# Optimization experiments

Measured on AMD Instinct MI355X. Metric: run time of the kernel, lower is better.

Reference implementation:

```python
import jax, jax.numpy as jnp
from jax import lax
import numpy as np

POOLED_H = 7
POOLED_W = 7
SPATIAL_SCALE = 0.0625


def setup_inputs() -> dict:
    key = jax.random.key(0)
    kf, kx1, ky1, kw, kh = jax.random.split(key, 5)
    B, H, W, C = 1, 64, 64, 512
    N = 512
    img_h, img_w = H / SPATIAL_SCALE, W / SPATIAL_SCALE
    feat = jax.random.normal(kf, (B, H, W, C), dtype=jnp.float32)
    # rois: (batch_idx, x1, y1, x2, y2) in image coordinates, boxes inside image
    x1 = jax.random.uniform(kx1, (N,), minval=0.0, maxval=img_w * 0.8)
    y1 = jax.random.uniform(ky1, (N,), minval=0.0, maxval=img_h * 0.8)
    bw = jax.random.uniform(kw, (N,), minval=16.0, maxval=img_w * 0.5)
    bh = jax.random.uniform(kh, (N,), minval=16.0, maxval=img_h * 0.5)
    x2 = jnp.clip(x1 + bw, 0.0, img_w - 1.0)
    y2 = jnp.clip(y1 + bh, 0.0, img_h - 1.0)
    bidx = jnp.zeros((N,), dtype=jnp.float32)
    rois = jnp.stack([bidx, x1, y1, x2, y2], axis=1).astype(jnp.float32)
    return {"feat": feat, "rois": rois}


def _roi_pool(feat, rois, pooled_h, pooled_w, spatial_scale):
    B, H, W, C = feat.shape
    N = rois.shape[0]
    # max extent of a single bin (Caffe: hend-hstart <= bin_size + 2 <= H/pooled_h + 2)
    MBH = int(np.ceil(H / pooled_h)) + 2
    MBW = int(np.ceil(W / pooled_w)) + 2

    roi_batch = rois[:, 0].astype(jnp.int32)
    start_w = jnp.round(rois[:, 1] * spatial_scale).astype(jnp.int32)
    start_h = jnp.round(rois[:, 2] * spatial_scale).astype(jnp.int32)
    end_w = jnp.round(rois[:, 3] * spatial_scale).astype(jnp.int32)
    end_h = jnp.round(rois[:, 4] * spatial_scale).astype(jnp.int32)
    roi_h = jnp.maximum(end_h - start_h + 1, 1).astype(jnp.float32)
    roi_w = jnp.maximum(end_w - start_w + 1, 1).astype(jnp.float32)
    bin_h = roi_h / pooled_h  # [N] float
    bin_w = roi_w / pooled_w

    ar_h = jnp.arange(MBH)
    ar_w = jnp.arange(MBW)

    def pool_one_bin(bin_idx):
        ph = bin_idx // pooled_w
        pw = bin_idx % pooled_w

        def per_roi(b, sh, sw, bh_, bw_):
            hstart = jnp.clip(jnp.floor(ph * bh_).astype(jnp.int32) + sh, 0, H)
            hend = jnp.clip(jnp.ceil((ph + 1) * bh_).astype(jnp.int32) + sh, 0, H)
            wstart = jnp.clip(jnp.floor(pw * bw_).astype(jnp.int32) + sw, 0, W)
            wend = jnp.clip(jnp.ceil((pw + 1) * bw_).astype(jnp.int32) + sw, 0, W)
            empty = (hend <= hstart) | (wend <= wstart)
            # fixed-size window covering the bin; clamp start so slice stays in-bounds
            s_h = jnp.clip(hstart, 0, H - MBH)
            s_w = jnp.clip(wstart, 0, W - MBW)
            fmap = lax.dynamic_index_in_dim(feat, b, axis=0, keepdims=False)  # [H,W,C]
            patch = lax.dynamic_slice(fmap, (s_h, s_w, 0), (MBH, MBW, C))  # [MBH,MBW,C]
            rows = s_h + ar_h
            cols = s_w + ar_w
            valid = ((rows >= hstart) & (rows < hend))[:, None] & ((cols >= wstart) & (cols < wend))[None, :]
            neg = jnp.array(-jnp.inf, patch.dtype)
            mx = jnp.max(jnp.where(valid[:, :, None], patch, neg), axis=(0, 1))  # [C]
            return jnp.where(empty, jnp.zeros_like(mx), mx)

        return jax.vmap(per_roi)(roi_batch, start_h, start_w, bin_h, bin_w)  # [N,C]

    out = lax.map(pool_one_bin, jnp.arange(pooled_h * pooled_w))  # [PH*PW, N, C]
    out = out.transpose(1, 0, 2).reshape(N, pooled_h, pooled_w, C)
    return out


def reference(feat, rois):
    return _roi_pool(feat, rois, POOLED_H, POOLED_W, SPATIAL_SCALE)
```

## Files before the change

kernel.cpp:

```cpp
#include <hip/hip_runtime.h>
#include <cmath>

#define PH 7
#define PW 7
#define FH 64
#define FW 64
#define CC 512
#define SCALE 0.0625f

typedef float f32x4 __attribute__((ext_vector_type(4)));

static __device__ __forceinline__ f32x4 vmax4(f32x4 a, f32x4 b) {
    f32x4 r;
    r.x = fmaxf(a.x, b.x); r.y = fmaxf(a.y, b.y);
    r.z = fmaxf(a.z, b.z); r.w = fmaxf(a.w, b.w);
    return r;
}

__global__ __launch_bounds__(512) void sort_rois_kernel(
        const float* __restrict__ rois, int N, int* __restrict__ perm) {
    __shared__ int base[64];
    __shared__ int cur[64];
    int t = threadIdx.x;
    if (t < 64) { base[t] = 0; cur[t] = 0; }
    __syncthreads();
    int b = -1;
    if (t < N) {
        const float* r = rois + (size_t)t * 5;
        int sh = (int)rintf(r[2] * SCALE);
        b = min(max(sh, 0), FH - 1);
        atomicAdd(&base[b], 1);
    }
    __syncthreads();
    if (t == 0) {
        int acc = 0;
        for (int i = 0; i < 64; ++i) { int c = base[i]; base[i] = acc; acc += c; }
    }
    __syncthreads();
    if (t < N) {
        int pos = base[b] + atomicAdd(&cur[b], 1);
        perm[pos] = t;
    }
}

__global__ __launch_bounds__(256) void roi_pool_kernel(
        const float* __restrict__ feat,
        const float* __restrict__ rois,
        const int* __restrict__ perm,
        float* __restrict__ out,
        int nBins) {
    int p = blockIdx.x;
    int nwg = gridDim.x;
    int q = nwg >> 3, rr = nwg & 7;
    int xcd = p & 7, o = p >> 3;
    int L = (xcd < rr ? xcd * (q + 1) : rr * (q + 1) + (xcd - rr) * q) + o;

    int tid = L * 256 + (int)threadIdx.x;
    int bin = tid >> 6;
    int lane = tid & 63;
    if (bin >= nBins) return;

    int s   = bin / (PH * PW);
    int rem = bin - s * (PH * PW);
    int ph  = rem / PW;
    int pw  = rem - ph * PW;
    int n   = perm[s];

    const float* r = rois + (size_t)n * 5;
    int bidx = (int)r[0];
    int sw = (int)rintf(r[1] * SCALE);
    int sh = (int)rintf(r[2] * SCALE);
    int ew = (int)rintf(r[3] * SCALE);
    int eh = (int)rintf(r[4] * SCALE);

    float roi_h = fmaxf((float)(eh - sh + 1), 1.0f);
    float roi_w = fmaxf((float)(ew - sw + 1), 1.0f);
    float bh = roi_h * (1.0f / 7.0f);
    float bw = roi_w * (1.0f / 7.0f);

    int hstart = min(max((int)floorf((float)ph * bh) + sh, 0), FH);
    int hend   = min(max((int)ceilf((float)(ph + 1) * bh) + sh, 0), FH);
    int wstart = min(max((int)floorf((float)pw * bw) + sw, 0), FW);
    int wend   = min(max((int)ceilf((float)(pw + 1) * bw) + sw, 0), FW);
    bool empty = (hend <= hstart) || (wend <= wstart);

    f32x4 mxA = { -INFINITY, -INFINITY, -INFINITY, -INFINITY };
    f32x4 mxB = mxA;

    if (!empty) {
        const int W = wend - wstart;
        int cells = (hend - hstart) * W;
        const float* ptr = feat + (size_t)bidx * (FH * FW * CC)
                         + (size_t)hstart * (FW * CC) + (size_t)wstart * CC
                         + (size_t)lane * 4;
        const int stepWrap = (FW - W + 1) * CC;
        int cw = W;

#define ADV() do { if (--cw == 0) { ptr += stepWrap; cw = W; } else ptr += CC; } while (0)

        while (cells >= 4) {
            const float* q0 = ptr; ADV();
            const float* q1 = ptr; ADV();
            const float* q2 = ptr; ADV();
            const float* q3 = ptr; ADV();
            f32x4 a0 = *(const f32x4*)q0;        f32x4 b0 = *(const f32x4*)(q0 + 256);
            f32x4 a1 = *(const f32x4*)q1;        f32x4 b1 = *(const f32x4*)(q1 + 256);
            f32x4 a2 = *(const f32x4*)q2;        f32x4 b2 = *(const f32x4*)(q2 + 256);
            f32x4 a3 = *(const f32x4*)q3;        f32x4 b3 = *(const f32x4*)(q3 + 256);
            a0 = vmax4(a0, a1); a2 = vmax4(a2, a3);
            b0 = vmax4(b0, b1); b2 = vmax4(b2, b3);
            mxA = vmax4(mxA, vmax4(a0, a2));
            mxB = vmax4(mxB, vmax4(b0, b2));
            cells -= 4;
        }
        while (cells > 0) {
            const float* q0 = ptr; ADV();
            f32x4 a0 = *(const f32x4*)q0;
            f32x4 b0 = *(const f32x4*)(q0 + 256);
            mxA = vmax4(mxA, a0);
            mxB = vmax4(mxB, b0);
            --cells;
        }
#undef ADV
    } else {
        mxA = (f32x4){0.f, 0.f, 0.f, 0.f};
        mxB = mxA;
    }

    float* op = out + ((size_t)n * (PH * PW) + rem) * CC + (size_t)lane * 4;
    __builtin_nontemporal_store(mxA, (f32x4*)op);
    __builtin_nontemporal_store(mxB, (f32x4*)(op + 256));
}

extern "C" void kernel_launch(void* const* d_in, const int* in_sizes, int n_in,
                              void* d_out, int out_size, void* d_ws, size_t ws_size,
                              hipStream_t stream) {
    const float* feat = (const float*)d_in[0];
    const float* rois = (const float*)d_in[1];
    float* out = (float*)d_out;
    int* perm = (int*)d_ws;

    int N = in_sizes[1] / 5;
    sort_rois_kernel<<<1, 512, 0, stream>>>(rois, N, perm);

    int nBins = N * PH * PW;
    int totalThreads = nBins * 64;
    int block = 256;
    int grid = (totalThreads + block - 1) / block;
    roi_pool_kernel<<<grid, block, 0, stream>>>(feat, rois, perm, out, nBins);
}
```

Baseline: 33.79 us.

## Precompute packed ROI geometry in sort kernel and unify tail loop with scalar offsets

The sort kernel now computes bin sizes and start coordinates once per ROI and writes them as a packed float4 in sorted order. This removes the dependent perm-then-rois lookup and the repeated rounding math from every bin wavefront. The pooling loop now uses wave-uniform scalar offsets via readfirstlane and a single quad loop. Tail cells are handled by redundantly reloading cell 0 rather than running a separate remainder loop. This trades a few extra loads on ragged tails for less scalar/vector address arithmetic and fewer branches, and relies on sh, sw and bidx fitting the bit fields.

```diff
diff --git a/kernel.cpp b/kernel.cpp
--- a/kernel.cpp
+++ b/kernel.cpp
@@ -18,16 +18,24 @@
 }
 
 __global__ __launch_bounds__(512) void sort_rois_kernel(
-        const float* __restrict__ rois, int N, int* __restrict__ perm) {
+        const float* __restrict__ rois, int N, float4* __restrict__ geo) {
     __shared__ int base[64];
     __shared__ int cur[64];
     int t = threadIdx.x;
     if (t < 64) { base[t] = 0; cur[t] = 0; }
     __syncthreads();
-    int b = -1;
+    int b = -1, packed = 0;
+    float bh = 0.f, bw = 0.f;
     if (t < N) {
         const float* r = rois + (size_t)t * 5;
+        int bidx = (int)r[0];
+        int sw = (int)rintf(r[1] * SCALE);
         int sh = (int)rintf(r[2] * SCALE);
+        int ew = (int)rintf(r[3] * SCALE);
+        int eh = (int)rintf(r[4] * SCALE);
+        bh = fmaxf((float)(eh - sh + 1), 1.0f) * (1.0f / 7.0f);
+        bw = fmaxf((float)(ew - sw + 1), 1.0f) * (1.0f / 7.0f);
+        packed = t | (sh << 10) | (sw << 17) | (bidx << 24);
         b = min(max(sh, 0), FH - 1);
         atomicAdd(&base[b], 1);
     }
@@ -39,14 +47,15 @@
     __syncthreads();
     if (t < N) {
         int pos = base[b] + atomicAdd(&cur[b], 1);
-        perm[pos] = t;
+        float4 g;
+        g.x = bh; g.y = bw; g.z = __int_as_float(packed); g.w = 0.f;
+        geo[pos] = g;
     }
 }
 
 __global__ __launch_bounds__(256) void roi_pool_kernel(
         const float* __restrict__ feat,
-        const float* __restrict__ rois,
-        const int* __restrict__ perm,
+        const float4* __restrict__ geo,
         float* __restrict__ out,
         int nBins) {
     int p = blockIdx.x;
@@ -64,62 +73,62 @@
     int rem = bin - s * (PH * PW);
     int ph  = rem / PW;
     int pw  = rem - ph * PW;
-    int n   = perm[s];
 
-    const float* r = rois + (size_t)n * 5;
-    int bidx = (int)r[0];
-    int sw = (int)rintf(r[1] * SCALE);
-    int sh = (int)rintf(r[2] * SCALE);
-    int ew = (int)rintf(r[3] * SCALE);
-    int eh = (int)rintf(r[4] * SCALE);
-
-    float roi_h = fmaxf((float)(eh - sh + 1), 1.0f);
-    float roi_w = fmaxf((float)(ew - sw + 1), 1.0f);
-    float bh = roi_h * (1.0f / 7.0f);
-    float bw = roi_w * (1.0f / 7.0f);
+    float4 g = geo[s];
+    float bh = g.x, bw = g.y;
+    int packed = __float_as_int(g.z);
+    int n    = packed & 1023;
+    int sh   = (packed >> 10) & 127;
+    int sw   = (packed >> 17) & 127;
+    int bidx = (packed >> 24) & 255;
 
     int hstart = min(max((int)floorf((float)ph * bh) + sh, 0), FH);
     int hend   = min(max((int)ceilf((float)(ph + 1) * bh) + sh, 0), FH);
     int wstart = min(max((int)floorf((float)pw * bw) + sw, 0), FW);
     int wend   = min(max((int)ceilf((float)(pw + 1) * bw) + sw, 0), FW);
-    bool empty = (hend <= hstart) || (wend <= wstart);
+
+    int Wn = wend - wstart;
+    int Hn = hend - hstart;
+    bool empty = (Hn <= 0) || (Wn <= 0);
 
     f32x4 mxA = { -INFINITY, -INFINITY, -INFINITY, -INFINITY };
     f32x4 mxB = mxA;
 
     if (!empty) {
-        const int W = wend - wstart;
-        int cells = (hend - hstart) * W;
-        const float* ptr = feat + (size_t)bidx * (FH * FW * CC)
-                         + (size_t)hstart * (FW * CC) + (size_t)wstart * CC
-                         + (size_t)lane * 4;
-        const int stepWrap = (FW - W + 1) * CC;
-        int cw = W;
+        unsigned cells = (unsigned)__builtin_amdgcn_readfirstlane(Hn * Wn);
+        unsigned Wu    = (unsigned)__builtin_amdgcn_readfirstlane(Wn);
+        unsigned wrap  = (unsigned)__builtin_amdgcn_readfirstlane((FW - Wn + 1) * CC);
+        unsigned off0  = (unsigned)__builtin_amdgcn_readfirstlane(
+            (bidx * FH * FW + hstart * FW + wstart) * CC);
 
-#define ADV() do { if (--cw == 0) { ptr += stepWrap; cw = W; } else ptr += CC; } while (0)
+        const float* fb = feat + off0;
+        unsigned vo = (unsigned)lane * 4;
 
-        while (cells >= 4) {
-            const float* q0 = ptr; ADV();
-            const float* q1 = ptr; ADV();
-            const float* q2 = ptr; ADV();
-            const float* q3 = ptr; ADV();
-            f32x4 a0 = *(const f32x4*)q0;        f32x4 b0 = *(const f32x4*)(q0 + 256);
-            f32x4 a1 = *(const f32x4*)q1;        f32x4 b1 = *(const f32x4*)(q1 + 256);
-            f32x4 a2 = *(const f32x4*)q2;        f32x4 b2 = *(const f32x4*)(q2 + 256);
-            f32x4 a3 = *(const f32x4*)q3;        f32x4 b3 = *(const f32x4*)(q3 + 256);
+        unsigned soff = 0;
+        unsigned cw = Wu;
+        unsigned c = 0;
+        unsigned quads = (cells + 3) >> 2;
+
+#define ADV() do { if (--cw == 0) { soff += wrap; cw = Wu; } else soff += CC; } while (0)
+
+        for (; quads; --quads) {
+            unsigned o0 = soff;                          ADV();
+            unsigned o1 = (c + 1 < cells) ? soff : 0u;   ADV();
+            unsigned o2 = (c + 2 < cells) ? soff : 0u;   ADV();
+            unsigned o3 = (c + 3 < cells) ? soff : 0u;   ADV();
+            c += 4;
+            const float* p0 = fb + o0;
+            const float* p1 = fb + o1;
+            const float* p2 = fb + o2;
+            const float* p3 = fb + o3;
+            f32x4 a0 = *(const f32x4*)(p0 + vo);  f32x4 b0 = *(const f32x4*)(p0 + vo + 256);
+            f32x4 a1 = *(const f32x4*)(p1 + vo);  f32x4 b1 = *(const f32x4*)(p1 + vo + 256);
+            f32x4 a2 = *(const f32x4*)(p2 + vo);  f32x4 b2 = *(const f32x4*)(p2 + vo + 256);
+            f32x4 a3 = *(const f32x4*)(p3 + vo);  f32x4 b3 = *(const f32x4*)(p3 + vo + 256);
             a0 = vmax4(a0, a1); a2 = vmax4(a2, a3);
             b0 = vmax4(b0, b1); b2 = vmax4(b2, b3);
             mxA = vmax4(mxA, vmax4(a0, a2));
             mxB = vmax4(mxB, vmax4(b0, b2));
-            cells -= 4;
-        }
-        while (cells > 0) {
-            const float* q0 = ptr; ADV();
-            f32x4 a0 = *(const f32x4*)q0;
-            f32x4 b0 = *(const f32x4*)(q0 + 256);
-            mxA = vmax4(mxA, a0);
-            mxB = vmax4(mxB, b0);
-            --cells;
         }
 #undef ADV
     } else {
@@ -138,14 +147,14 @@
     const float* feat = (const float*)d_in[0];
     const float* rois = (const float*)d_in[1];
     float* out = (float*)d_out;
-    int* perm = (int*)d_ws;
+    float4* geo = (float4*)d_ws;
 
     int N = in_sizes[1] / 5;
-    sort_rois_kernel<<<1, 512, 0, stream>>>(rois, N, perm);
+    sort_rois_kernel<<<1, 512, 0, stream>>>(rois, N, geo);
 
     int nBins = N * PH * PW;
     int totalThreads = nBins * 64;
     int block = 256;
     int grid = (totalThreads + block - 1) / block;
-    roi_pool_kernel<<<grid, block, 0, stream>>>(feat, rois, perm, out, nBins);
+    roi_pool_kernel<<<grid, block, 0, stream>>>(feat, geo, out, nBins);
 }
```

Result: no change. 34.35 us (+1.7%).

## Precompute ROI geometry in sort kernel and split each bin across two waves

Applied to the files above, without the earlier changes.

The sort kernel now computes each ROI's bin sizes and packed start/index fields and writes them as a float4 in sorted order. The pool kernel reads this instead of doing an indirect perm lookup and recomputing the geometry. Each bin is now covered by two wavefronts, one per 256-channel half, which doubles the wave count. The main loop is unrolled to 8 cells to keep enough loads in flight per wave. This adds more parallelism and less serial work per wave, at the cost of duplicated index math and twice as many waves to schedule.

```diff
diff --git a/kernel.cpp b/kernel.cpp
--- a/kernel.cpp
+++ b/kernel.cpp
@@ -18,16 +18,24 @@
 }
 
 __global__ __launch_bounds__(512) void sort_rois_kernel(
-        const float* __restrict__ rois, int N, int* __restrict__ perm) {
+        const float* __restrict__ rois, int N, float4* __restrict__ geo) {
     __shared__ int base[64];
     __shared__ int cur[64];
     int t = threadIdx.x;
     if (t < 64) { base[t] = 0; cur[t] = 0; }
     __syncthreads();
-    int b = -1;
+    int b = -1, packed = 0;
+    float bh = 0.f, bw = 0.f;
     if (t < N) {
         const float* r = rois + (size_t)t * 5;
+        int bidx = (int)r[0];
+        int sw = (int)rintf(r[1] * SCALE);
         int sh = (int)rintf(r[2] * SCALE);
+        int ew = (int)rintf(r[3] * SCALE);
+        int eh = (int)rintf(r[4] * SCALE);
+        bh = fmaxf((float)(eh - sh + 1), 1.0f) * (1.0f / 7.0f);
+        bw = fmaxf((float)(ew - sw + 1), 1.0f) * (1.0f / 7.0f);
+        packed = t | (sh << 10) | (sw << 17) | (bidx << 24);
         b = min(max(sh, 0), FH - 1);
         atomicAdd(&base[b], 1);
     }
@@ -39,44 +47,41 @@
     __syncthreads();
     if (t < N) {
         int pos = base[b] + atomicAdd(&cur[b], 1);
-        perm[pos] = t;
+        float4 g;
+        g.x = bh; g.y = bw; g.z = __int_as_float(packed); g.w = 0.f;
+        geo[pos] = g;
     }
 }
 
 __global__ __launch_bounds__(256) void roi_pool_kernel(
         const float* __restrict__ feat,
-        const float* __restrict__ rois,
-        const int* __restrict__ perm,
+        const float4* __restrict__ geo,
         float* __restrict__ out,
         int nBins) {
-    int p = blockIdx.x;
-    int nwg = gridDim.x;
+    int p = blockIdx.x, nwg = gridDim.x;
     int q = nwg >> 3, rr = nwg & 7;
     int xcd = p & 7, o = p >> 3;
     int L = (xcd < rr ? xcd * (q + 1) : rr * (q + 1) + (xcd - rr) * q) + o;
 
     int tid = L * 256 + (int)threadIdx.x;
-    int bin = tid >> 6;
+    int wv   = tid >> 6;
     int lane = tid & 63;
+    int bin  = wv >> 1;
+    int half = wv & 1;
     if (bin >= nBins) return;
 
     int s   = bin / (PH * PW);
     int rem = bin - s * (PH * PW);
     int ph  = rem / PW;
     int pw  = rem - ph * PW;
-    int n   = perm[s];
 
-    const float* r = rois + (size_t)n * 5;
-    int bidx = (int)r[0];
-    int sw = (int)rintf(r[1] * SCALE);
-    int sh = (int)rintf(r[2] * SCALE);
-    int ew = (int)rintf(r[3] * SCALE);
-    int eh = (int)rintf(r[4] * SCALE);
-
-    float roi_h = fmaxf((float)(eh - sh + 1), 1.0f);
-    float roi_w = fmaxf((float)(ew - sw + 1), 1.0f);
-    float bh = roi_h * (1.0f / 7.0f);
-    float bw = roi_w * (1.0f / 7.0f);
+    float4 g = geo[s];
+    float bh = g.x, bw = g.y;
+    int packed = __float_as_int(g.z);
+    int n    = packed & 1023;
+    int sh   = (packed >> 10) & 127;
+    int sw   = (packed >> 17) & 127;
+    int bidx = (packed >> 24) & 255;
 
     int hstart = min(max((int)floorf((float)ph * bh) + sh, 0), FH);
     int hend   = min(max((int)ceilf((float)(ph + 1) * bh) + sh, 0), FH);
@@ -84,52 +89,60 @@
     int wend   = min(max((int)ceilf((float)(pw + 1) * bw) + sw, 0), FW);
     bool empty = (hend <= hstart) || (wend <= wstart);
 
-    f32x4 mxA = { -INFINITY, -INFINITY, -INFINITY, -INFINITY };
-    f32x4 mxB = mxA;
+    f32x4 mx = { -INFINITY, -INFINITY, -INFINITY, -INFINITY };
 
     if (!empty) {
         const int W = wend - wstart;
         int cells = (hend - hstart) * W;
         const float* ptr = feat + (size_t)bidx * (FH * FW * CC)
                          + (size_t)hstart * (FW * CC) + (size_t)wstart * CC
-                         + (size_t)lane * 4;
+                         + (size_t)(half * 256 + lane * 4);
         const int stepWrap = (FW - W + 1) * CC;
         int cw = W;
 
 #define ADV() do { if (--cw == 0) { ptr += stepWrap; cw = W; } else ptr += CC; } while (0)
 
-        while (cells >= 4) {
+        while (cells >= 8) {
             const float* q0 = ptr; ADV();
             const float* q1 = ptr; ADV();
             const float* q2 = ptr; ADV();
             const float* q3 = ptr; ADV();
-            f32x4 a0 = *(const f32x4*)q0;        f32x4 b0 = *(const f32x4*)(q0 + 256);
-            f32x4 a1 = *(const f32x4*)q1;        f32x4 b1 = *(const f32x4*)(q1 + 256);
-            f32x4 a2 = *(const f32x4*)q2;        f32x4 b2 = *(const f32x4*)(q2 + 256);
-            f32x4 a3 = *(const f32x4*)q3;        f32x4 b3 = *(const f32x4*)(q3 + 256);
+            const float* q4 = ptr; ADV();
+            const float* q5 = ptr; ADV();
+            const float* q6 = ptr; ADV();
+            const float* q7 = ptr; ADV();
+            f32x4 a0 = *(const f32x4*)q0; f32x4 a1 = *(const f32x4*)q1;
+            f32x4 a2 = *(const f32x4*)q2; f32x4 a3 = *(const f32x4*)q3;
+            f32x4 a4 = *(const f32x4*)q4; f32x4 a5 = *(const f32x4*)q5;
+            f32x4 a6 = *(const f32x4*)q6; f32x4 a7 = *(const f32x4*)q7;
             a0 = vmax4(a0, a1); a2 = vmax4(a2, a3);
-            b0 = vmax4(b0, b1); b2 = vmax4(b2, b3);
-            mxA = vmax4(mxA, vmax4(a0, a2));
-            mxB = vmax4(mxB, vmax4(b0, b2));
+            a4 = vmax4(a4, a5); a6 = vmax4(a6, a7);
+            mx = vmax4(mx, vmax4(vmax4(a0, a2), vmax4(a4, a6)));
+            cells -= 8;
+        }
+        if (cells >= 4) {
+            const float* q0 = ptr; ADV();
+            const float* q1 = ptr; ADV();
+            const float* q2 = ptr; ADV();
+            const float* q3 = ptr; ADV();
+            f32x4 a0 = *(const f32x4*)q0; f32x4 a1 = *(const f32x4*)q1;
+            f32x4 a2 = *(const f32x4*)q2; f32x4 a3 = *(const f32x4*)q3;
+            mx = vmax4(mx, vmax4(vmax4(a0, a1), vmax4(a2, a3)));
             cells -= 4;
         }
         while (cells > 0) {
             const float* q0 = ptr; ADV();
-            f32x4 a0 = *(const f32x4*)q0;
-            f32x4 b0 = *(const f32x4*)(q0 + 256);
-            mxA = vmax4(mxA, a0);
-            mxB = vmax4(mxB, b0);
+            mx = vmax4(mx, *(const f32x4*)q0);
             --cells;
         }
 #undef ADV
     } else {
-        mxA = (f32x4){0.f, 0.f, 0.f, 0.f};
-        mxB = mxA;
+        mx = (f32x4){0.f, 0.f, 0.f, 0.f};
     }
 
-    float* op = out + ((size_t)n * (PH * PW) + rem) * CC + (size_t)lane * 4;
-    __builtin_nontemporal_store(mxA, (f32x4*)op);
-    __builtin_nontemporal_store(mxB, (f32x4*)(op + 256));
+    float* op = out + ((size_t)n * (PH * PW) + rem) * CC
+              + (size_t)(half * 256 + lane * 4);
+    __builtin_nontemporal_store(mx, (f32x4*)op);
 }
 
 extern "C" void kernel_launch(void* const* d_in, const int* in_sizes, int n_in,
@@ -138,14 +151,14 @@
     const float* feat = (const float*)d_in[0];
     const float* rois = (const float*)d_in[1];
     float* out = (float*)d_out;
-    int* perm = (int*)d_ws;
+    float4* geo = (float4*)d_ws;
 
     int N = in_sizes[1] / 5;
-    sort_rois_kernel<<<1, 512, 0, stream>>>(rois, N, perm);
+    sort_rois_kernel<<<1, 512, 0, stream>>>(rois, N, geo);
 
     int nBins = N * PH * PW;
-    int totalThreads = nBins * 64;
+    int totalThreads = nBins * 2 * 64;
     int block = 256;
     int grid = (totalThreads + block - 1) / block;
-    roi_pool_kernel<<<grid, block, 0, stream>>>(feat, rois, perm, out, nBins);
+    roi_pool_kernel<<<grid, block, 0, stream>>>(feat, geo, out, nBins);
 }
```

New measurement: 32.70 us. -3.2%, faster.
